# Performance work log

Measured on AMD Instinct MI355X. Metric: run time of the kernel, lower is better.

The kernel has to match this reference:

```python
import jax, jax.numpy as jnp
import numpy as np
from jax import lax

SEQ, IN, H, NC, L = 2048, 1024, 1024, 512, 3


def _lstm_layer(x_seq, W_ih, W_hh, b_ih, b_hh):
    # x_seq: [T, in] -> hs: [T, H]. PyTorch gate order: i, f, g, o.
    Hd = W_hh.shape[1]
    # Precompute input contribution for all timesteps (one big GEMM).
    gx = x_seq @ W_ih.T + (b_ih + b_hh)  # [T, 4H]

    def step(carry, gx_t):
        h, c = carry
        gates = gx_t + h @ W_hh.T  # [4H]
        i, f, g, o = jnp.split(gates, 4)
        i = jax.nn.sigmoid(i)
        f = jax.nn.sigmoid(f)
        g = jnp.tanh(g)
        o = jax.nn.sigmoid(o)
        c = f * c + i * g
        h = o * jnp.tanh(c)
        return (h, c), h

    h0 = jnp.zeros((Hd,), x_seq.dtype)
    c0 = jnp.zeros((Hd,), x_seq.dtype)
    _, hs = lax.scan(step, (h0, c0), gx)
    return hs


def setup_inputs() -> dict:
    key = jax.random.key(0)
    ks = jax.random.split(key, 16)
    s = 1.0 / np.sqrt(H)  # PyTorch LSTM init scale
    d = {"x": jax.random.normal(ks[0], (SEQ, IN), jnp.float32)}
    i = 1
    for l in range(L):
        in_dim = IN if l == 0 else H
        d[f"W_ih_{l}"] = jax.random.normal(ks[i], (4 * H, in_dim), jnp.float32) * s; i += 1
        d[f"W_hh_{l}"] = jax.random.normal(ks[i], (4 * H, H), jnp.float32) * s; i += 1
        d[f"b_ih_{l}"] = jax.random.normal(ks[i], (4 * H,), jnp.float32) * s; i += 1
        d[f"b_hh_{l}"] = jax.random.normal(ks[i], (4 * H,), jnp.float32) * s; i += 1
    d["fc_w"] = jax.random.normal(ks[13], (NC, H), jnp.float32) * s
    d["fc_b"] = jax.random.normal(ks[14], (NC,), jnp.float32) * s
    return d


def reference(x, W_ih_0, W_hh_0, b_ih_0, b_hh_0,
              W_ih_1, W_hh_1, b_ih_1, b_hh_1,
              W_ih_2, W_hh_2, b_ih_2, b_hh_2,
              fc_w, fc_b):
    h = _lstm_layer(x, W_ih_0, W_hh_0, b_ih_0, b_hh_0)
    h = _lstm_layer(h, W_ih_1, W_hh_1, b_ih_1, b_hh_1)
    h = _lstm_layer(h, W_ih_2, W_hh_2, b_ih_2, b_hh_2)
    return h @ fc_w.T + fc_b  # [SEQ, NC]
```

## Files before the change

kernel.cpp:

```cpp
#include <hip/hip_runtime.h>

#define HDIM  1024
#define FOURH 4096
#define TSEQ  2048
#define NCLS  512

#define SCANB  64
#define GEMMB  32
#define U16    16
#define DRING  128
#define GXRING 128
#define CHUNK  64
#define NCHUNK 32

#define CNT0 0
#define CNT1 64
#define CD0  128
#define CD1  192
#define SP1  256
#define SP2  320
#define SYNC_BYTES 2048
#define HDR_BYTES 32768

union SharedU {
    struct { float h[HDIM]; float gate[4][U16]; } scan;
    struct { float As[16][72]; float Bs[16][132]; } gemm;
};

__device__ __forceinline__ unsigned long long ald(const unsigned long long* p) {
    return __hip_atomic_load(p, __ATOMIC_RELAXED, __HIP_MEMORY_SCOPE_AGENT);
}
__device__ __forceinline__ void ast(unsigned long long* p, unsigned long long v) {
    __hip_atomic_store(p, v, __ATOMIC_RELAXED, __HIP_MEMORY_SCOPE_AGENT);
}
__device__ __forceinline__ unsigned ald32(const unsigned* p) {
    return __hip_atomic_load(p, __ATOMIC_RELAXED, __HIP_MEMORY_SCOPE_AGENT);
}
__device__ __forceinline__ void ast32(unsigned* p, unsigned v) {
    __hip_atomic_store(p, v, __ATOMIC_RELAXED, __HIP_MEMORY_SCOPE_AGENT);
}

__global__ __launch_bounds__(256) void gemm_bias_kernel(
    const float* __restrict__ A, const float* __restrict__ B,
    const float* __restrict__ bias1, const float* __restrict__ bias2,
    float* __restrict__ C, int M, int N, int K)
{
    __shared__ float As[16][68];
    __shared__ float Bs[16][68];

    const int tid = threadIdx.x;
    const int tx = tid & 15;
    const int ty = tid >> 4;
    const int n0 = blockIdx.x * 64;
    const int m0 = blockIdx.y * 64;
    const int r  = tid >> 2;
    const int kq = tid & 3;

    float acc[4][4];
#pragma unroll
    for (int i = 0; i < 4; ++i)
#pragma unroll
        for (int j = 0; j < 4; ++j) acc[i][j] = 0.f;

    for (int k0 = 0; k0 < K; k0 += 16) {
        float4 va = *(const float4*)&A[(size_t)(m0 + r) * K + k0 + 4 * kq];
        float4 vb = *(const float4*)&B[(size_t)(n0 + r) * K + k0 + 4 * kq];
        As[4 * kq + 0][r] = va.x; As[4 * kq + 1][r] = va.y;
        As[4 * kq + 2][r] = va.z; As[4 * kq + 3][r] = va.w;
        Bs[4 * kq + 0][r] = vb.x; Bs[4 * kq + 1][r] = vb.y;
        Bs[4 * kq + 2][r] = vb.z; Bs[4 * kq + 3][r] = vb.w;
        __syncthreads();
#pragma unroll
        for (int kk = 0; kk < 16; ++kk) {
            float4 a = *(const float4*)&As[kk][4 * ty];
            float4 b = *(const float4*)&Bs[kk][4 * tx];
            acc[0][0] = fmaf(a.x, b.x, acc[0][0]);
            acc[0][1] = fmaf(a.x, b.y, acc[0][1]);
            acc[0][2] = fmaf(a.x, b.z, acc[0][2]);
            acc[0][3] = fmaf(a.x, b.w, acc[0][3]);
            acc[1][0] = fmaf(a.y, b.x, acc[1][0]);
            acc[1][1] = fmaf(a.y, b.y, acc[1][1]);
            acc[1][2] = fmaf(a.y, b.z, acc[1][2]);
            acc[1][3] = fmaf(a.y, b.w, acc[1][3]);
            acc[2][0] = fmaf(a.z, b.x, acc[2][0]);
            acc[2][1] = fmaf(a.z, b.y, acc[2][1]);
            acc[2][2] = fmaf(a.z, b.z, acc[2][2]);
            acc[2][3] = fmaf(a.z, b.w, acc[2][3]);
            acc[3][0] = fmaf(a.w, b.x, acc[3][0]);
            acc[3][1] = fmaf(a.w, b.y, acc[3][1]);
            acc[3][2] = fmaf(a.w, b.z, acc[3][2]);
            acc[3][3] = fmaf(a.w, b.w, acc[3][3]);
        }
        __syncthreads();
    }

    float4 bv = *(const float4*)&bias1[n0 + 4 * tx];
    if (bias2) {
        float4 b2 = *(const float4*)&bias2[n0 + 4 * tx];
        bv.x += b2.x; bv.y += b2.y; bv.z += b2.z; bv.w += b2.w;
    }
#pragma unroll
    for (int i = 0; i < 4; ++i) {
        const int row = m0 + 4 * ty + i;
        float4 o;
        o.x = acc[i][0] + bv.x;
        o.y = acc[i][1] + bv.y;
        o.z = acc[i][2] + bv.z;
        o.w = acc[i][3] + bv.w;
        *(float4*)&C[(size_t)row * N + n0 + 4 * tx] = o;
    }
}

#define LOAD_GX(T) do { if (lane < 32) {                                      \
    const int g_ = lane >> 3, up_ = lane & 7;                                 \
    const unsigned long long pk_ = ald(gxb +                                  \
        (((size_t)((T) & gxmask)) * FOURH + g_ * HDIM + u0 + 2 * up_) / 2);   \
    gxlo = __uint_as_float((unsigned)pk_);                                    \
    gxhi = __uint_as_float((unsigned)(pk_ >> 32)); } } while (0)

__device__ void scan_role(int bi,
    const float* __restrict__ Whh,
    const unsigned long long* __restrict__ gxb, unsigned gxmask,
    unsigned long long* __restrict__ ring,
    const unsigned* cdSrc,
    const unsigned* cdBp,
    unsigned* sp,
    float* __restrict__ h2,
    SharedU* sm)
{
    const int tid  = threadIdx.x;
    const int w    = tid >> 6;
    const int lane = tid & 63;
    const int g    = w & 3;
    const int ub   = (w >> 2) * 8;
    const int u0   = bi * U16;

    float4 wv[8][4];
#pragma unroll
    for (int u = 0; u < 8; ++u) {
        const float* Wr = Whh + (size_t)(g * HDIM + u0 + ub + u) * HDIM;
#pragma unroll
        for (int j = 0; j < 4; ++j)
            wv[u][j] = *(const float4*)(Wr + 256 * j + 4 * lane);
    }
    { float2 z = {0.f, 0.f}; *(float2*)(sm->scan.h + 2 * tid) = z; }
    float cst = 0.f;
    float gxlo = 0.f, gxhi = 0.f;
    __syncthreads();

    for (int t = 0; t < TSEQ; ++t) {
        if (w == 0) {
            if ((t & (CHUNK - 1)) == 0) {
                if (cdSrc && lane == 0) {
                    const unsigned need = (unsigned)(t >> 6) + 1u;
                    while (ald32(cdSrc) < need) __builtin_amdgcn_s_sleep(4);
                }
                LOAD_GX(t);
            }
            if (cdBp && t >= DRING && lane == 0) {
                const unsigned need = (unsigned)((t - DRING) >> 6) + 1u;
                while (ald32(cdBp) < need) __builtin_amdgcn_s_sleep(4);
            }
        }

        float4 hv[4];
#pragma unroll
        for (int j = 0; j < 4; ++j)
            hv[j] = *(const float4*)(sm->scan.h + 256 * j + 4 * lane);
        float acc[8];
#pragma unroll
        for (int u = 0; u < 8; ++u) {
            float a = 0.f;
#pragma unroll
            for (int j = 0; j < 4; ++j) {
                a = fmaf(wv[u][j].x, hv[j].x, a);
                a = fmaf(wv[u][j].y, hv[j].y, a);
                a = fmaf(wv[u][j].z, hv[j].z, a);
                a = fmaf(wv[u][j].w, hv[j].w, a);
            }
            acc[u] = a;
        }
#pragma unroll
        for (int off = 32; off; off >>= 1)
#pragma unroll
            for (int u = 0; u < 8; ++u)
                acc[u] += __shfl_xor(acc[u], off, 64);
        if (lane == 0)
#pragma unroll
            for (int u = 0; u < 8; ++u) sm->scan.gate[g][ub + u] = acc[u];
        __syncthreads();

        const unsigned tag = (unsigned)(t + 1);
        if (w == 0) {
            const int src = (lane & 15) >> 1;
            float gv[4];
#pragma unroll
            for (int gg = 0; gg < 4; ++gg) {
                const float a = __shfl(gxlo, 8 * gg + src, 64);
                const float b = __shfl(gxhi, 8 * gg + src, 64);
                gv[gg] = (lane & 1) ? b : a;
            }
            if (lane < U16) {
                const float gi = sm->scan.gate[0][lane] + gv[0];
                const float gf = sm->scan.gate[1][lane] + gv[1];
                const float gg_ = sm->scan.gate[2][lane] + gv[2];
                const float go = sm->scan.gate[3][lane] + gv[3];
                const float si = 1.f / (1.f + __expf(-gi));
                const float sf = 1.f / (1.f + __expf(-gf));
                const float tg = tanhf(gg_);
                const float so = 1.f / (1.f + __expf(-go));
                cst = sf * cst + si * tg;
                const float h = so * tanhf(cst);
                ast(ring + (size_t)(t & (DRING - 1)) * HDIM + u0 + lane,
                    ((unsigned long long)tag << 32) |
                    (unsigned long long)__float_as_uint(h));
                if (h2) h2[(size_t)t * HDIM + u0 + lane] = h;
            }
            if (sp && bi == 0 && lane == 0) ast32(sp, (unsigned)t);
            if (((t + 1) & (CHUNK - 1)) != 0 && t + 1 < TSEQ) LOAD_GX(t + 1);
        }

        if (t + 1 < TSEQ) {
            const unsigned long long* hb = ring + (size_t)(t & (DRING - 1)) * HDIM;
            unsigned long long v0 = 0, v1 = 0;
            bool got0 = false, got1 = false;
            while (!(got0 && got1)) {
                if (!got0) {
                    const unsigned long long x = ald(hb + 2 * tid);
                    if ((unsigned)(x >> 32) == tag) { v0 = x; got0 = true; }
                }
                if (!got1) {
                    const unsigned long long x = ald(hb + 2 * tid + 1);
                    if ((unsigned)(x >> 32) == tag) { v1 = x; got1 = true; }
                }
                if (!(got0 && got1)) __builtin_amdgcn_s_sleep(1);
            }
            sm->scan.h[2 * tid]     = __uint_as_float((unsigned)v0);
            sm->scan.h[2 * tid + 1] = __uint_as_float((unsigned)v1);
            __syncthreads();
        }
    }
}

__device__ void gemm_role(int tix,
    const unsigned long long* __restrict__ ringS,
    const float* __restrict__ Wih,
    const float* __restrict__ bih, const float* __restrict__ bhh,
    float* __restrict__ gxr,
    unsigned* cnt, unsigned* cd, const unsigned* spC,
    SharedU* sm)
{
    const int tid = threadIdx.x;
    const int tx = tid & 31, ty = tid >> 5;
    const int n0 = tix * 128;
    const int tt = tid >> 3, ke = tid & 7;
    const int cB = tid >> 2, kq = tid & 3;

    float4 bv;
    {
        const float4 b1 = *(const float4*)(bih + n0 + 4 * tx);
        const float4 b2 = *(const float4*)(bhh + n0 + 4 * tx);
        bv.x = b1.x + b2.x; bv.y = b1.y + b2.y;
        bv.z = b1.z + b2.z; bv.w = b1.w + b2.w;
    }
    unsigned long long* gxr64 = (unsigned long long*)gxr;

    for (int q = 0; q < NCHUNK; ++q) {
        if (q >= GXRING / CHUNK && tid == 0) {
            const unsigned need = (unsigned)((q - GXRING / CHUNK + 1) * CHUNK + 2);
            while (ald32(spC) < need) __builtin_amdgcn_s_sleep(8);
        }
        __syncthreads();

        float acc[4][4];
#pragma unroll
        for (int i = 0; i < 4; ++i)
#pragma unroll
            for (int j = 0; j < 4; ++j) acc[i][j] = 0.f;

        for (int k0 = 0; k0 < HDIM; k0 += 16) {
            {
                const int trow = q * CHUNK + tt;
                const unsigned expt = (unsigned)(trow + 1);
                const unsigned long long* srcp =
                    ringS + (size_t)(trow & (DRING - 1)) * HDIM + k0 + 2 * ke;
#pragma unroll
                for (int e = 0; e < 2; ++e) {
                    unsigned long long x;
                    while ((unsigned)((x = ald(srcp + e)) >> 32) != expt)
                        __builtin_amdgcn_s_sleep(1);
                    sm->gemm.As[2 * ke + e][tt] = __uint_as_float((unsigned)x);
                }
            }
            {
                const float4 vb = *(const float4*)(Wih + (size_t)(n0 + cB) * HDIM + k0 + 4 * kq);
                sm->gemm.Bs[4 * kq + 0][cB] = vb.x;
                sm->gemm.Bs[4 * kq + 1][cB] = vb.y;
                sm->gemm.Bs[4 * kq + 2][cB] = vb.z;
                sm->gemm.Bs[4 * kq + 3][cB] = vb.w;
            }
            __syncthreads();
#pragma unroll
            for (int kk = 0; kk < 16; ++kk) {
                const float4 a = *(const float4*)&sm->gemm.As[kk][4 * ty];
                const float4 b = *(const float4*)&sm->gemm.Bs[kk][4 * tx];
                acc[0][0] = fmaf(a.x, b.x, acc[0][0]);
                acc[0][1] = fmaf(a.x, b.y, acc[0][1]);
                acc[0][2] = fmaf(a.x, b.z, acc[0][2]);
                acc[0][3] = fmaf(a.x, b.w, acc[0][3]);
                acc[1][0] = fmaf(a.y, b.x, acc[1][0]);
                acc[1][1] = fmaf(a.y, b.y, acc[1][1]);
                acc[1][2] = fmaf(a.y, b.z, acc[1][2]);
                acc[1][3] = fmaf(a.y, b.w, acc[1][3]);
                acc[2][0] = fmaf(a.z, b.x, acc[2][0]);
                acc[2][1] = fmaf(a.z, b.y, acc[2][1]);
                acc[2][2] = fmaf(a.z, b.z, acc[2][2]);
                acc[2][3] = fmaf(a.z, b.w, acc[2][3]);
                acc[3][0] = fmaf(a.w, b.x, acc[3][0]);
                acc[3][1] = fmaf(a.w, b.y, acc[3][1]);
                acc[3][2] = fmaf(a.w, b.z, acc[3][2]);
                acc[3][3] = fmaf(a.w, b.w, acc[3][3]);
            }
            __syncthreads();
        }

#pragma unroll
        for (int i = 0; i < 4; ++i) {
            const int trow = q * CHUNK + 4 * ty + i;
            const float o0 = acc[i][0] + bv.x;
            const float o1 = acc[i][1] + bv.y;
            const float o2 = acc[i][2] + bv.z;
            const float o3 = acc[i][3] + bv.w;
            const size_t base =
                ((size_t)(trow & (GXRING - 1)) * FOURH + n0 + 4 * tx) / 2;
            ast(gxr64 + base,
                ((unsigned long long)__float_as_uint(o1) << 32) | __float_as_uint(o0));
            ast(gxr64 + base + 1,
                ((unsigned long long)__float_as_uint(o3) << 32) | __float_as_uint(o2));
        }
        asm volatile("s_waitcnt vmcnt(0)" ::: "memory");
        __syncthreads();
        if (tid == 0) {
            const unsigned old = __hip_atomic_fetch_add(cnt + q, 1u,
                                     __ATOMIC_RELAXED, __HIP_MEMORY_SCOPE_AGENT);
            if (old + 1u == (unsigned)GEMMB) ast32(cd, (unsigned)(q + 1));
        }
    }
}

__global__ __launch_bounds__(512) void fused_scan(
    const float* __restrict__ gx0,
    const float* __restrict__ Whh0, const float* __restrict__ Whh1,
    const float* __restrict__ Whh2,
    const float* __restrict__ Wih1, const float* __restrict__ Wih2,
    const float* __restrict__ bih1, const float* __restrict__ bhh1,
    const float* __restrict__ bih2, const float* __restrict__ bhh2,
    unsigned long long* ring0, unsigned long long* ring1, unsigned long long* ring2,
    float* gxr1, float* gxr2,
    float* h2out, unsigned* syncw)
{
    __shared__ SharedU sm;
    const int lb = blockIdx.x;
    if (lb < 3 * SCANB) {
        const int layer = lb >> 6;
        const int bi    = lb & 63;
        if (layer == 0)
            scan_role(bi, Whh0, (const unsigned long long*)gx0, 2047u, ring0,
                      nullptr, syncw + CD0, nullptr, nullptr, &sm);
        else if (layer == 1)
            scan_role(bi, Whh1, (const unsigned long long*)gxr1, GXRING - 1u, ring1,
                      syncw + CD0, syncw + CD1, syncw + SP1, nullptr, &sm);
        else
            scan_role(bi, Whh2, (const unsigned long long*)gxr2, GXRING - 1u, ring2,
                      syncw + CD1, nullptr, syncw + SP2, h2out, &sm);
    } else {
        const int gb  = lb - 3 * SCANB;
        const int gl  = gb >> 5;
        const int tix = gb & 31;
        if (gl == 0)
            gemm_role(tix, ring0, Wih1, bih1, bhh1, gxr1,
                      syncw + CNT0, syncw + CD0, syncw + SP1, &sm);
        else
            gemm_role(tix, ring1, Wih2, bih2, bhh2, gxr2,
                      syncw + CNT1, syncw + CD1, syncw + SP2, &sm);
    }
}

extern "C" void kernel_launch(void* const* d_in, const int* in_sizes, int n_in,
                              void* d_out, int out_size, void* d_ws, size_t ws_size,
                              hipStream_t stream)
{
    (void)in_sizes; (void)n_in; (void)out_size; (void)ws_size;

    const float* x = (const float*)d_in[0];
    const float* W_ih[3] = {(const float*)d_in[1], (const float*)d_in[5], (const float*)d_in[9]};
    const float* W_hh[3] = {(const float*)d_in[2], (const float*)d_in[6], (const float*)d_in[10]};
    const float* b_ih[3] = {(const float*)d_in[3], (const float*)d_in[7], (const float*)d_in[11]};
    const float* b_hh[3] = {(const float*)d_in[4], (const float*)d_in[8], (const float*)d_in[12]};
    const float* fc_w = (const float*)d_in[13];
    const float* fc_b = (const float*)d_in[14];
    float* out = (float*)d_out;

    unsigned* syncw = (unsigned*)d_ws;
    float* gx = (float*)((char*)d_ws + HDR_BYTES);
    float* A  = gx + (size_t)TSEQ * FOURH;
    unsigned long long* ring0 = (unsigned long long*)(A + (size_t)TSEQ * HDIM);
    unsigned long long* ring1 = ring0 + (size_t)DRING * HDIM;
    unsigned long long* ring2 = ring1 + (size_t)DRING * HDIM;
    float* gxr1 = (float*)(ring2 + (size_t)DRING * HDIM);
    float* gxr2 = gxr1 + (size_t)GXRING * FOURH;

    hipMemsetAsync(syncw, 0, SYNC_BYTES, stream);

    {
        dim3 g(FOURH / 64, TSEQ / 64);
        gemm_bias_kernel<<<g, 256, 0, stream>>>(x, W_ih[0], b_ih[0], b_hh[0],
                                                gx, TSEQ, FOURH, HDIM);
    }

    {
        const float* gx0_c = gx;
        float* h2 = A;
        void* args[] = {
            (void*)&gx0_c,
            (void*)&W_hh[0], (void*)&W_hh[1], (void*)&W_hh[2],
            (void*)&W_ih[1], (void*)&W_ih[2],
            (void*)&b_ih[1], (void*)&b_hh[1],
            (void*)&b_ih[2], (void*)&b_hh[2],
            (void*)&ring0, (void*)&ring1, (void*)&ring2,
            (void*)&gxr1, (void*)&gxr2,
            (void*)&h2, (void*)&syncw
        };
        hipLaunchCooperativeKernel((void*)fused_scan,
                                   dim3(3 * SCANB + 2 * GEMMB), dim3(512),
                                   args, 0, stream);
    }

    {
        dim3 g(NCLS / 64, TSEQ / 64);
        gemm_bias_kernel<<<g, 256, 0, stream>>>(A, fc_w, fc_b, nullptr,
                                                out, TSEQ, NCLS, HDIM);
    }
}
```

Before: 8.067 ms.

## Replace per-element tagged h ring with packed floats plus per-block tag flags

The h ring now stores two floats per 64-bit word with no embedded tag. Each scan block publishes a per-block monotonic tag after waiting for its stores to complete. Consumers, both scan blocks and gemm blocks, spin on 64 tag words and then do a single plain load each, instead of polling tagged words one by one. This halves ring traffic and cuts the number of spinning loads. It relies on the vmcnt wait giving enough memory ordering for the relaxed atomics, and it also swaps tanhf for an exp-based tanh.

```diff
diff --git a/kernel.cpp b/kernel.cpp
--- a/kernel.cpp
+++ b/kernel.cpp
@@ -19,7 +19,11 @@
 #define CD1  192
 #define SP1  256
 #define SP2  320
-#define SYNC_BYTES 2048
+#define TAGSTRIDE 16
+#define TAGS0 1024
+#define TAGS1 2048
+#define TAGS2 3072
+#define SYNC_BYTES 16384
 #define HDR_BYTES 32768
 
 union SharedU {
@@ -39,6 +43,9 @@
 __device__ __forceinline__ void ast32(unsigned* p, unsigned v) {
     __hip_atomic_store(p, v, __ATOMIC_RELAXED, __HIP_MEMORY_SCOPE_AGENT);
 }
+
+__device__ __forceinline__ float fsig(float x)  { return 1.f / (1.f + __expf(-x)); }
+__device__ __forceinline__ float ftanh(float x) { return 1.f - 2.f / (1.f + __expf(2.f * x)); }
 
 __global__ __launch_bounds__(256) void gemm_bias_kernel(
     const float* __restrict__ A, const float* __restrict__ B,
@@ -122,6 +129,7 @@
     const float* __restrict__ Whh,
     const unsigned long long* __restrict__ gxb, unsigned gxmask,
     unsigned long long* __restrict__ ring,
+    unsigned* tags,
     const unsigned* cdSrc,
     const unsigned* cdBp,
     unsigned* sp,
@@ -200,43 +208,41 @@
                 const float b = __shfl(gxhi, 8 * gg + src, 64);
                 gv[gg] = (lane & 1) ? b : a;
             }
+            float hval = 0.f;
             if (lane < U16) {
                 const float gi = sm->scan.gate[0][lane] + gv[0];
                 const float gf = sm->scan.gate[1][lane] + gv[1];
                 const float gg_ = sm->scan.gate[2][lane] + gv[2];
                 const float go = sm->scan.gate[3][lane] + gv[3];
-                const float si = 1.f / (1.f + __expf(-gi));
-                const float sf = 1.f / (1.f + __expf(-gf));
-                const float tg = tanhf(gg_);
-                const float so = 1.f / (1.f + __expf(-go));
+                const float si = fsig(gi);
+                const float sf = fsig(gf);
+                const float tg = ftanh(gg_);
+                const float so = fsig(go);
                 cst = sf * cst + si * tg;
-                const float h = so * tanhf(cst);
-                ast(ring + (size_t)(t & (DRING - 1)) * HDIM + u0 + lane,
-                    ((unsigned long long)tag << 32) |
-                    (unsigned long long)__float_as_uint(h));
-                if (h2) h2[(size_t)t * HDIM + u0 + lane] = h;
-            }
-            if (sp && bi == 0 && lane == 0) ast32(sp, (unsigned)t);
+                hval = so * ftanh(cst);
+                if (h2) h2[(size_t)t * HDIM + u0 + lane] = hval;
+            }
+            const float hodd = __shfl(hval, lane | 1, 64);
+            if (lane < U16 && !(lane & 1))
+                ast(ring + (size_t)(t & (DRING - 1)) * (HDIM / 2) + ((u0 + lane) >> 1),
+                    ((unsigned long long)__float_as_uint(hodd) << 32) |
+                    (unsigned long long)__float_as_uint(hval));
+            asm volatile("s_waitcnt vmcnt(0)" ::: "memory");
+            if (lane == 0) {
+                ast32(tags + (size_t)bi * TAGSTRIDE, tag);
+                if (sp && bi == 0) ast32(sp, (unsigned)t);
+            }
             if (((t + 1) & (CHUNK - 1)) != 0 && t + 1 < TSEQ) LOAD_GX(t + 1);
         }
 
         if (t + 1 < TSEQ) {
-            const unsigned long long* hb = ring + (size_t)(t & (DRING - 1)) * HDIM;
-            unsigned long long v0 = 0, v1 = 0;
-            bool got0 = false, got1 = false;
-            while (!(got0 && got1)) {
-                if (!got0) {
-                    const unsigned long long x = ald(hb + 2 * tid);
-                    if ((unsigned)(x >> 32) == tag) { v0 = x; got0 = true; }
-                }
-                if (!got1) {
-                    const unsigned long long x = ald(hb + 2 * tid + 1);
-                    if ((unsigned)(x >> 32) == tag) { v1 = x; got1 = true; }
-                }
-                if (!(got0 && got1)) __builtin_amdgcn_s_sleep(1);
-            }
-            sm->scan.h[2 * tid]     = __uint_as_float((unsigned)v0);
-            sm->scan.h[2 * tid + 1] = __uint_as_float((unsigned)v1);
+            const unsigned* tp = tags + (size_t)(tid >> 3) * TAGSTRIDE;
+            while (ald32(tp) < tag) {  }
+            const unsigned long long v =
+                ald(ring + (size_t)(t & (DRING - 1)) * (HDIM / 2) + tid);
+            *(float2*)(sm->scan.h + 2 * tid) =
+                make_float2(__uint_as_float((unsigned)v),
+                            __uint_as_float((unsigned)(v >> 32)));
             __syncthreads();
         }
     }
@@ -244,6 +250,7 @@
 
 __device__ void gemm_role(int tix,
     const unsigned long long* __restrict__ ringS,
+    const unsigned* __restrict__ tagsSrc,
     const float* __restrict__ Wih,
     const float* __restrict__ bih, const float* __restrict__ bhh,
     float* __restrict__ gxr,
@@ -270,6 +277,11 @@
             const unsigned need = (unsigned)((q - GXRING / CHUNK + 1) * CHUNK + 2);
             while (ald32(spC) < need) __builtin_amdgcn_s_sleep(8);
         }
+        if (tid < 64) {
+            const unsigned need = (unsigned)((q + 1) * CHUNK);
+            const unsigned* tp = tagsSrc + (size_t)tid * TAGSTRIDE;
+            while (ald32(tp) < need) __builtin_amdgcn_s_sleep(4);
+        }
         __syncthreads();
 
         float acc[4][4];
@@ -281,16 +293,10 @@
         for (int k0 = 0; k0 < HDIM; k0 += 16) {
             {
                 const int trow = q * CHUNK + tt;
-                const unsigned expt = (unsigned)(trow + 1);
-                const unsigned long long* srcp =
-                    ringS + (size_t)(trow & (DRING - 1)) * HDIM + k0 + 2 * ke;
-#pragma unroll
-                for (int e = 0; e < 2; ++e) {
-                    unsigned long long x;
-                    while ((unsigned)((x = ald(srcp + e)) >> 32) != expt)
-                        __builtin_amdgcn_s_sleep(1);
-                    sm->gemm.As[2 * ke + e][tt] = __uint_as_float((unsigned)x);
-                }
+                const unsigned long long x =
+                    ald(ringS + (size_t)(trow & (DRING - 1)) * (HDIM / 2) + (k0 >> 1) + ke);
+                sm->gemm.As[2 * ke + 0][tt] = __uint_as_float((unsigned)x);
+                sm->gemm.As[2 * ke + 1][tt] = __uint_as_float((unsigned)(x >> 32));
             }
             {
                 const float4 vb = *(const float4*)(Wih + (size_t)(n0 + cB) * HDIM + k0 + 4 * kq);
@@ -360,28 +366,31 @@
     float* h2out, unsigned* syncw)
 {
     __shared__ SharedU sm;
+    unsigned* tags0 = syncw + TAGS0;
+    unsigned* tags1 = syncw + TAGS1;
+    unsigned* tags2 = syncw + TAGS2;
     const int lb = blockIdx.x;
     if (lb < 3 * SCANB) {
         const int layer = lb >> 6;
         const int bi    = lb & 63;
         if (layer == 0)
-            scan_role(bi, Whh0, (const unsigned long long*)gx0, 2047u, ring0,
+            scan_role(bi, Whh0, (const unsigned long long*)gx0, 2047u, ring0, tags0,
                       nullptr, syncw + CD0, nullptr, nullptr, &sm);
         else if (layer == 1)
-            scan_role(bi, Whh1, (const unsigned long long*)gxr1, GXRING - 1u, ring1,
+            scan_role(bi, Whh1, (const unsigned long long*)gxr1, GXRING - 1u, ring1, tags1,
                       syncw + CD0, syncw + CD1, syncw + SP1, nullptr, &sm);
         else
-            scan_role(bi, Whh2, (const unsigned long long*)gxr2, GXRING - 1u, ring2,
+            scan_role(bi, Whh2, (const unsigned long long*)gxr2, GXRING - 1u, ring2, tags2,
                       syncw + CD1, nullptr, syncw + SP2, h2out, &sm);
     } else {
         const int gb  = lb - 3 * SCANB;
         const int gl  = gb >> 5;
         const int tix = gb & 31;
         if (gl == 0)
-            gemm_role(tix, ring0, Wih1, bih1, bhh1, gxr1,
+            gemm_role(tix, ring0, tags0, Wih1, bih1, bhh1, gxr1,
                       syncw + CNT0, syncw + CD0, syncw + SP1, &sm);
         else
-            gemm_role(tix, ring1, Wih2, bih2, bhh2, gxr2,
+            gemm_role(tix, ring1, tags1, Wih2, bih2, bhh2, gxr2,
                       syncw + CNT1, syncw + CD1, syncw + SP2, &sm);
     }
 }
@@ -405,9 +414,9 @@
     float* gx = (float*)((char*)d_ws + HDR_BYTES);
     float* A  = gx + (size_t)TSEQ * FOURH;
     unsigned long long* ring0 = (unsigned long long*)(A + (size_t)TSEQ * HDIM);
-    unsigned long long* ring1 = ring0 + (size_t)DRING * HDIM;
-    unsigned long long* ring2 = ring1 + (size_t)DRING * HDIM;
-    float* gxr1 = (float*)(ring2 + (size_t)DRING * HDIM);
+    unsigned long long* ring1 = ring0 + (size_t)DRING * (HDIM / 2);
+    unsigned long long* ring2 = ring1 + (size_t)DRING * (HDIM / 2);
+    float* gxr1 = (float*)(ring2 + (size_t)DRING * (HDIM / 2));
     float* gxr2 = gxr1 + (size_t)GXRING * FOURH;
 
     hipMemsetAsync(syncw, 0, SYNC_BYTES, stream);
```

New measurement: 8.697 ms. +7.8%, slower.

## Replace per-step block barrier with per-quarter LDS flags in LSTM scan

Applied to the files above, without the earlier changes.

Each step of the recurrent scan used to end with a block-wide barrier after the hidden state was copied from the ring into shared memory. That barrier is replaced by four shared-memory counters, one per 256-element quarter, bumped by each pair of waves once its slice is written. The matvec now waits on each quarter's counter just before reading it, so compute on early quarters can start while other waves are still polling the global ring. The activation step moves from wave 0 to wave 7 and uses an exp-based tanh instead of tanhf; this cuts latency on the serial path but adds spin-waiting on LDS and relies on hand-placed waitcnt for correctness.

```diff
diff --git a/kernel.cpp b/kernel.cpp
--- a/kernel.cpp
+++ b/kernel.cpp
@@ -39,6 +39,9 @@
 __device__ __forceinline__ void ast32(unsigned* p, unsigned v) {
     __hip_atomic_store(p, v, __ATOMIC_RELAXED, __HIP_MEMORY_SCOPE_AGENT);
 }
+
+__device__ __forceinline__ float fsig(float x)  { return 1.f / (1.f + __expf(-x)); }
+__device__ __forceinline__ float ftanh(float x) { return 1.f - 2.f / (1.f + __expf(2.f * x)); }
 
 __global__ __launch_bounds__(256) void gemm_bias_kernel(
     const float* __restrict__ A, const float* __restrict__ B,
@@ -126,7 +129,7 @@
     const unsigned* cdBp,
     unsigned* sp,
     float* __restrict__ h2,
-    SharedU* sm)
+    SharedU* sm, unsigned* qflag)
 {
     const int tid  = threadIdx.x;
     const int w    = tid >> 6;
@@ -144,12 +147,13 @@
             wv[u][j] = *(const float4*)(Wr + 256 * j + 4 * lane);
     }
     { float2 z = {0.f, 0.f}; *(float2*)(sm->scan.h + 2 * tid) = z; }
+    if (tid < 4) qflag[tid] = 0u;
     float cst = 0.f;
     float gxlo = 0.f, gxhi = 0.f;
     __syncthreads();
 
     for (int t = 0; t < TSEQ; ++t) {
-        if (w == 0) {
+        if (w == 7) {
             if ((t & (CHUNK - 1)) == 0) {
                 if (cdSrc && lane == 0) {
                     const unsigned need = (unsigned)(t >> 6) + 1u;
@@ -163,22 +167,26 @@
             }
         }
 
-        float4 hv[4];
-#pragma unroll
-        for (int j = 0; j < 4; ++j)
-            hv[j] = *(const float4*)(sm->scan.h + 256 * j + 4 * lane);
         float acc[8];
 #pragma unroll
-        for (int u = 0; u < 8; ++u) {
-            float a = 0.f;
-#pragma unroll
-            for (int j = 0; j < 4; ++j) {
-                a = fmaf(wv[u][j].x, hv[j].x, a);
-                a = fmaf(wv[u][j].y, hv[j].y, a);
-                a = fmaf(wv[u][j].z, hv[j].z, a);
-                a = fmaf(wv[u][j].w, hv[j].w, a);
-            }
-            acc[u] = a;
+        for (int u = 0; u < 8; ++u) acc[u] = 0.f;
+#pragma unroll
+        for (int j = 0; j < 4; ++j) {
+            if (t) {
+                const unsigned need = 2u * (unsigned)t;
+                while (__hip_atomic_load(qflag + j, __ATOMIC_RELAXED,
+                                         __HIP_MEMORY_SCOPE_WORKGROUP) < need) {}
+                asm volatile("s_waitcnt lgkmcnt(0)" ::: "memory");
+                __builtin_amdgcn_sched_barrier(0);
+            }
+            const float4 hvj = *(const float4*)(sm->scan.h + 256 * j + 4 * lane);
+#pragma unroll
+            for (int u = 0; u < 8; ++u) {
+                acc[u] = fmaf(wv[u][j].x, hvj.x, acc[u]);
+                acc[u] = fmaf(wv[u][j].y, hvj.y, acc[u]);
+                acc[u] = fmaf(wv[u][j].z, hvj.z, acc[u]);
+                acc[u] = fmaf(wv[u][j].w, hvj.w, acc[u]);
+            }
         }
 #pragma unroll
         for (int off = 32; off; off >>= 1)
@@ -191,7 +199,7 @@
         __syncthreads();
 
         const unsigned tag = (unsigned)(t + 1);
-        if (w == 0) {
+        if (w == 7) {
             const int src = (lane & 15) >> 1;
             float gv[4];
 #pragma unroll
@@ -205,12 +213,12 @@
                 const float gf = sm->scan.gate[1][lane] + gv[1];
                 const float gg_ = sm->scan.gate[2][lane] + gv[2];
                 const float go = sm->scan.gate[3][lane] + gv[3];
-                const float si = 1.f / (1.f + __expf(-gi));
-                const float sf = 1.f / (1.f + __expf(-gf));
-                const float tg = tanhf(gg_);
-                const float so = 1.f / (1.f + __expf(-go));
+                const float si = fsig(gi);
+                const float sf = fsig(gf);
+                const float tg = ftanh(gg_);
+                const float so = fsig(go);
                 cst = sf * cst + si * tg;
-                const float h = so * tanhf(cst);
+                const float h = so * ftanh(cst);
                 ast(ring + (size_t)(t & (DRING - 1)) * HDIM + u0 + lane,
                     ((unsigned long long)tag << 32) |
                     (unsigned long long)__float_as_uint(h));
@@ -237,7 +245,10 @@
             }
             sm->scan.h[2 * tid]     = __uint_as_float((unsigned)v0);
             sm->scan.h[2 * tid + 1] = __uint_as_float((unsigned)v1);
-            __syncthreads();
+            asm volatile("s_waitcnt lgkmcnt(0)" ::: "memory");
+            if (lane == 0)
+                __hip_atomic_fetch_add(qflag + (w >> 1), 1u, __ATOMIC_RELAXED,
+                                       __HIP_MEMORY_SCOPE_WORKGROUP);
         }
     }
 }
@@ -360,19 +371,20 @@
     float* h2out, unsigned* syncw)
 {
     __shared__ SharedU sm;
+    __shared__ unsigned qflag[4];
     const int lb = blockIdx.x;
     if (lb < 3 * SCANB) {
         const int layer = lb >> 6;
         const int bi    = lb & 63;
         if (layer == 0)
             scan_role(bi, Whh0, (const unsigned long long*)gx0, 2047u, ring0,
-                      nullptr, syncw + CD0, nullptr, nullptr, &sm);
+                      nullptr, syncw + CD0, nullptr, nullptr, &sm, qflag);
         else if (layer == 1)
             scan_role(bi, Whh1, (const unsigned long long*)gxr1, GXRING - 1u, ring1,
-                      syncw + CD0, syncw + CD1, syncw + SP1, nullptr, &sm);
+                      syncw + CD0, syncw + CD1, syncw + SP1, nullptr, &sm, qflag);
         else
             scan_role(bi, Whh2, (const unsigned long long*)gxr2, GXRING - 1u, ring2,
-                      syncw + CD1, nullptr, syncw + SP2, h2out, &sm);
+                      syncw + CD1, nullptr, syncw + SP2, h2out, &sm, qflag);
     } else {
         const int gb  = lb - 3 * SCANB;
         const int gl  = gb >> 5;
```

Result: no change. 8.066 ms (-0.0%).
